# Kernel tuning notes

Measured on AMD Instinct MI355X. Metric: run time of the kernel, lower is better.

The kernel has to match this reference:

```python
import jax, jax.numpy as jnp
import numpy as np

H, D = 4, 32            # heads, per-head dim
HD = H * D              # hidden_dim = output_dim = 128
ND, NG = 10000, 30000   # num disease / gene nodes
E_DG, E_GD, E_GG = 150000, 150000, 300000
L = 2                   # num HGTConv layers


def setup_inputs() -> dict:
    key = jax.random.key(0)
    ks = jax.random.split(key, 16)
    s = 0.05
    return {
        "x_d": jax.random.normal(ks[0], (ND, HD), jnp.float32),
        "x_g": jax.random.normal(ks[1], (NG, HD), jnp.float32),
        "src_dg": jax.random.randint(ks[2], (E_DG,), 0, ND),
        "dst_dg": jax.random.randint(ks[3], (E_DG,), 0, NG),
        "src_gd": jax.random.randint(ks[4], (E_GD,), 0, NG),
        "dst_gd": jax.random.randint(ks[5], (E_GD,), 0, ND),
        "src_gg": jax.random.randint(ks[6], (E_GG,), 0, NG),
        "dst_gg": jax.random.randint(ks[7], (E_GG,), 0, NG),
        # fused K/Q/V projection per node type, stacked over layers
        "Wkqv_d": jax.random.normal(ks[8], (L, HD, 3 * HD), jnp.float32) * s,
        "bkqv_d": jnp.zeros((L, 3 * HD), jnp.float32),
        "Wkqv_g": jax.random.normal(ks[9], (L, HD, 3 * HD), jnp.float32) * s,
        "bkqv_g": jnp.zeros((L, 3 * HD), jnp.float32),
        # output linear per node type
        "Wout_d": jax.random.normal(ks[10], (L, HD, HD), jnp.float32) * s,
        "bout_d": jnp.zeros((L, HD), jnp.float32),
        "Wout_g": jax.random.normal(ks[11], (L, HD, HD), jnp.float32) * s,
        "bout_g": jnp.zeros((L, HD), jnp.float32),
        # learnable skip gates per node type
        "skip_d": jnp.ones((L,), jnp.float32),
        "skip_g": jnp.ones((L,), jnp.float32),
        # per edge-type relation matrices (key, message) and priors, 3 edge types
        "arel": jax.random.normal(ks[12], (L, 3, H, D, D), jnp.float32) * s,
        "mrel": jax.random.normal(ks[13], (L, 3, H, D, D), jnp.float32) * s,
        "prel": jnp.ones((L, 3, H), jnp.float32),
    }


def _hgt_forward(x_d, x_g, src_dg, dst_dg, src_gd, dst_gd, src_gg, dst_gg,
                 Wkqv_d, bkqv_d, Wkqv_g, bkqv_g, Wout_d, bout_d, Wout_g, bout_g,
                 skip_d, skip_g, arel, mrel, prel):
    scale = 1.0 / (D ** 0.5)
    for l in range(L):
        def kqv(x, W, b):
            t = (x @ W + b).reshape(-1, 3, H, D)
            return t[:, 0], t[:, 1], t[:, 2]

        k_d, q_d, v_d = kqv(x_d, Wkqv_d[l], bkqv_d[l])
        k_g, q_g, v_g = kqv(x_g, Wkqv_g[l], bkqv_g[l])

        def edge_msgs(k_src, v_src, q_dst, src, dst, et):
            # gather src K/V, transform by per-edge-type relation matrices
            ke = jnp.einsum('ehd,hdf->ehf', k_src[src], arel[l, et])  # [E,H,D]
            ve = jnp.einsum('ehd,hdf->ehf', v_src[src], mrel[l, et])  # [E,H,D]
            a = jnp.sum(q_dst[dst] * ke, axis=-1) * prel[l, et] * scale  # [E,H]
            return a, ve

        a_dg, v_dg = edge_msgs(k_d, v_d, q_g, src_dg, dst_dg, 0)
        a_gd, v_gd = edge_msgs(k_g, v_g, q_d, src_gd, dst_gd, 1)
        a_gg, v_gg = edge_msgs(k_g, v_g, q_g, src_gg, dst_gg, 2)

        def aggregate(alphas, vals, dsts, n):
            # segment softmax over ALL incoming edges of a dst node (across edge types)
            a = jnp.concatenate(alphas, axis=0)
            v = jnp.concatenate(vals, axis=0)
            d = jnp.concatenate(dsts, axis=0)
            amax = jax.ops.segment_max(a, d, num_segments=n)
            ex = jnp.exp(a - amax[d])
            den = jax.ops.segment_sum(ex, d, num_segments=n)
            w = ex / den[d]
            out = jax.ops.segment_sum(w[:, :, None] * v, d, num_segments=n)
            return out.reshape(n, HD)

        agg_g = aggregate([a_dg, a_gg], [v_dg, v_gg], [dst_dg, dst_gg], NG)
        agg_d = aggregate([a_gd], [v_gd], [dst_gd], ND)

        def update(agg, x, Wout, bout, skip):
            o = jax.nn.gelu(agg) @ Wout + bout
            g = jax.nn.sigmoid(skip)
            return g * o + (1.0 - g) * x

        x_d = update(agg_d, x_d, Wout_d[l], bout_d[l], skip_d[l])
        x_g = update(agg_g, x_g, Wout_g[l], bout_g[l], skip_g[l])
    return x_d, x_g


def reference(x_d, x_g, src_dg, dst_dg, src_gd, dst_gd, src_gg, dst_gg,
              Wkqv_d, bkqv_d, Wkqv_g, bkqv_g, Wout_d, bout_d, Wout_g, bout_g,
              skip_d, skip_g, arel, mrel, prel):
    return _hgt_forward(x_d, x_g, src_dg, dst_dg, src_gd, dst_gd, src_gg, dst_gg,
                        Wkqv_d, bkqv_d, Wkqv_g, bkqv_g, Wout_d, bout_d, Wout_g, bout_g,
                        skip_d, skip_g, arel, mrel, prel)
```

## Files before the change

kernel.cpp:

```cpp
#include <hip/hip_runtime.h>
#include <hip/hip_bf16.h>

#define H 4
#define D 32
#define HD 128
#define ND 10000
#define NG 30000
#define E_DG 150000
#define E_GD 150000
#define E_GG 300000
#define NE (E_DG + E_GD + E_GG)
#define EG (E_DG + E_GG)
#define NLAYER 2
#define NBG 30
#define NBD 10
#define OCG 640
#define OCD 384
#define GOFF ((size_t)ND * OCD)
#define NSCAT 2344
#define NGEMM0 1250
#define XLSTRIDE 136

typedef _Float16 f16;
typedef __attribute__((ext_vector_type(2))) _Float16 f16x2;
typedef __attribute__((ext_vector_type(4))) _Float16 f16x4;
typedef __attribute__((ext_vector_type(8))) _Float16 f16x8;
typedef __attribute__((ext_vector_type(8))) unsigned short u16x8;
typedef __attribute__((ext_vector_type(4))) float f32x4;

__device__ __forceinline__ float bu(unsigned short u) {
    return __uint_as_float(((unsigned)u) << 16);
}
__device__ __forceinline__ float ldraw(const void* p, size_t i, bool isf32) {
    return isf32 ? ((const float*)p)[i] : bu(((const unsigned short*)p)[i]);
}
__device__ __forceinline__ float gelu(float v) {
    const float c = 0.79788456080286536f * (v + 0.044715f * v * v * v);
    return 0.5f * v * (1.0f + tanhf(c));
}

__device__ __forceinline__ void combine_one(
    int idx, int GENE, bool isf32,
    const void* W, const void* bvec,
    const void* arel, const void* mrel, const void* prel,
    f16* __restrict__ Wp, float* __restrict__ bp) {
    const int OC = GENE ? OCG : OCD;
    const int l = idx / (OC * 128);
    const int rem = idx - l * OC * 128;
    const int col = rem >> 7;
    const int d = rem & 127;
    const int g = col >> 7;
    const int jj = col & 127;
    const int h = jj >> 5, f = jj & 31;
    const size_t wbase = (size_t)l * 128 * 384;
    const size_t bbase = (size_t)l * 384;
    float val, bv = 0.f;
    if (g == 0) {
        val = ldraw(W, wbase + d * 384 + 128 + jj, isf32);
        bv = ldraw(bvec, bbase + 128 + jj, isf32);
    } else {
        const int et = GENE ? ((g <= 2) ? 1 : 2) : 0;
        const bool isk = (g & 1);
        const void* mat = isk ? arel : mrel;
        const size_t mbase = (((size_t)(l * 3 + et) * H + h) << 10) + f;
        const int sb = isk ? 0 : 256;
        val = 0.f;
        for (int dd = 0; dd < 32; dd++)
            val += ldraw(W, wbase + d * 384 + sb + h * 32 + dd, isf32) *
                   ldraw(mat, mbase + dd * 32, isf32);
        if (d == 0)
            for (int dd = 0; dd < 32; dd++)
                bv += ldraw(bvec, bbase + sb + h * 32 + dd, isf32) *
                      ldraw(mat, mbase + dd * 32, isf32);
        if (isk) {
            const float sc = ldraw(prel, (size_t)(l * 3 + et) * H + h, isf32) *
                             (0.17677669529663689f * 1.4426950408889634f);
            val *= sc;
            bv *= sc;
        }
    }
    Wp[(size_t)l * 4 * OC * 32 + ((size_t)(d >> 5) * OC + col) * 32 + (d & 31)] = (f16)val;
    if (d == 0) bp[l * OC + col] = bv;
}

__global__ __launch_bounds__(256) void k_prep0(
    const void* x0,
    const void* wkqvd_r, const void* bkqvd_r,
    const void* wkqvg_r, const void* bkqvg_r,
    const void* arel_r, const void* mrel_r, const void* prel_r,
    const void* woutd_r, const void* woutg_r,
    const void* boutd_r, const void* boutg_r,
    const void* skipd_r, const void* skipg_r,
    f16* __restrict__ Wp_d, float* __restrict__ bp_d,
    f16* __restrict__ Wp_g, float* __restrict__ bp_g,
    f16* __restrict__ Wpod, f16* __restrict__ Wpog,
    float* __restrict__ boutc_d, float* __restrict__ boutc_g,
    float* __restrict__ gates, int* __restrict__ flag,
    const int* __restrict__ dst_dg, const int* __restrict__ dst_gg,
    const int* __restrict__ dst_gd,
    int* __restrict__ cnt_g, int* __restrict__ cnt_d,
    int* __restrict__ rank, int* __restrict__ ready) {
    const int tid = threadIdx.x;
    const int b = blockIdx.x;
    if (b >= 1281) {
        const int i = (b - 1281) * 256 + tid;
        if (i < E_DG) rank[i] = atomicAdd(cnt_g + dst_dg[i], 1);
        else if (i < EG) rank[i] = atomicAdd(cnt_g + dst_gg[i - E_DG], 1);
        else if (i < NE) rank[i] = atomicAdd(cnt_d + dst_gd[i - EG], 1);
        return;
    }
    __shared__ int sbad;
    if (tid == 0) sbad = 0;
    __syncthreads();
    {
        const unsigned short* xs = (const unsigned short*)x0;
        int bad = 0;
        for (int i = tid; i < 1024; i += 256)
            if (!(fabsf(bu(xs[i])) < 1e6f)) bad = 1;
        if (bad) sbad = 1;
    }
    __syncthreads();
    const bool isf32 = (sbad != 0);

    if (b < 1280) {
        int idx = b * 256 + tid;
        const int nd = NLAYER * OCD * 128;
        const int ng = NLAYER * OCG * 128;
        const int np = 2 * NLAYER * 128 * 128;
        if (idx < nd) {
            combine_one(idx, 0, isf32, wkqvd_r, bkqvd_r, arel_r, mrel_r, prel_r, Wp_d, bp_d);
        } else if ((idx -= nd) < ng) {
            combine_one(idx, 1, isf32, wkqvg_r, bkqvg_r, arel_r, mrel_r, prel_r, Wp_g, bp_g);
        } else if ((idx -= ng) < np) {
            const int type = idx >= NLAYER * 128 * 128;
            int rem = idx - type * NLAYER * 128 * 128;
            const int l = rem / (128 * 128);
            rem -= l * 128 * 128;
            const int d = rem >> 7, col = rem & 127;
            const float w = ldraw(type ? woutg_r : woutd_r,
                                  (size_t)l * 128 * 128 + d * 128 + col, isf32);
            f16* out = (type ? Wpog : Wpod) +
                ((size_t)l * 4 + (d >> 5)) * 128 * 32 + col * 32 + (d & 31);
            *out = (f16)w;
        }
    } else {
        if (tid < NBG + NBD) ready[tid] = 0;
        if (tid == 0) {
            flag[0] = isf32 ? 1 : 0;
            gates[0] = 1.f / (1.f + expf(-ldraw(skipd_r, 0, isf32)));
            gates[1] = 1.f / (1.f + expf(-ldraw(skipg_r, 0, isf32)));
            gates[2] = 1.f / (1.f + expf(-ldraw(skipd_r, 1, isf32)));
            gates[3] = 1.f / (1.f + expf(-ldraw(skipg_r, 1, isf32)));
        }
        for (int i = tid; i < NLAYER * 128; i += 256) {
            boutc_d[i] = ldraw(boutd_r, i, isf32);
            boutc_g[i] = ldraw(boutg_r, i, isf32);
        }
    }
}

__global__ __launch_bounds__(256) void k_scan(
    const int* __restrict__ cnt_g, const int* __restrict__ cnt_d,
    int* __restrict__ ready,
    int* __restrict__ rp_g, int* __restrict__ rp_d) {
    const int b = blockIdx.x;
    const int tid = threadIdx.x;
    const bool isg = (b < NBG);
    const int* cnt = isg ? cnt_g : cnt_d;
    int* rp = isg ? rp_g : rp_d;
    const int n = isg ? NG : ND;
    const int lb = isg ? b : (b - NBG);
    const int i0 = lb * 1024 + tid * 4;
    int v[4];
    int t = 0;
#pragma unroll
    for (int j = 0; j < 4; j++) {
        v[j] = (i0 + j < n) ? cnt[i0 + j] : 0;
        t += v[j];
    }
    __shared__ int sdata[256];
    __shared__ int red2[256];
    __shared__ int s_off;
    sdata[tid] = t;
    __syncthreads();
    for (int d = 1; d < 256; d <<= 1) {
        const int u = (tid >= d) ? sdata[tid - d] : 0;
        __syncthreads();
        sdata[tid] += u;
        __syncthreads();
    }
    const int total = sdata[255];
    if (tid == 0) atomicExch(&ready[b], total + 1);
    const int p0 = isg ? 0 : NBG;
    const int npred = b - p0;
    int part = 0;
    for (int i = tid; i < npred; i += 256) {
        int vv;
        do { vv = atomicAdd(&ready[p0 + i], 0); } while (vv == 0);
        part += vv - 1;
    }
    red2[tid] = part;
    __syncthreads();
    for (int d = 128; d > 0; d >>= 1) {
        if (tid < d) red2[tid] += red2[tid + d];
        __syncthreads();
    }
    if (tid == 0) s_off = red2[0];
    __syncthreads();
    int run = s_off + sdata[tid] - t;
#pragma unroll
    for (int j = 0; j < 4; j++) {
        if (i0 + j < n) {
            run += v[j];
            rp[i0 + j + 1] = run;
        }
    }
    if (tid == 0 && lb == 0) rp[0] = 0;
}

__global__ __launch_bounds__(256) void k_scatter_gemm0(
    const int* __restrict__ src_dg, const int* __restrict__ dst_dg,
    const int* __restrict__ src_gg, const int* __restrict__ dst_gg,
    const int* __restrict__ src_gd, const int* __restrict__ dst_gd,
    const int* __restrict__ rp_g, const int* __restrict__ rp_d,
    const int* __restrict__ rank,
    int* __restrict__ edges_g, int* __restrict__ edges_d,
    const void* xd_r, const void* xg_r, const int* __restrict__ flag,
    const f16* __restrict__ Wpd, const float* __restrict__ bpd,
    const f16* __restrict__ Wpg, const float* __restrict__ bpg,
    f16* __restrict__ tab) {
    __shared__ f16 xls[32 * XLSTRIDE];
    if (blockIdx.x < NSCAT) {
        const int i = blockIdx.x * 256 + threadIdx.x;
        if (i < E_DG) {
            edges_g[rp_g[dst_dg[i]] + rank[i]] = src_dg[i] * OCD + 128;
        } else if (i < EG) {
            const int j = i - E_DG;
            edges_g[rp_g[dst_gg[j]] + rank[i]] = (int)GOFF + src_gg[j] * OCG + 384;
        } else if (i < NE) {
            const int j = i - EG;
            edges_d[rp_d[dst_gd[j]] + rank[i]] = (int)GOFF + src_gd[j] * OCG + 128;
        }
        return;
    }
    const bool isf32 = (*flag != 0);
    const int tid = threadIdx.x;
    const int mt0 = (blockIdx.x - NSCAT) * 2;
    for (int i = tid; i < 1024; i += 256) {
        const int row = i >> 5;
        const int c4 = (i & 31) * 4;
        const int gnode = mt0 * 16 + row;
        const bool gene = (gnode >= ND);
        const void* xr = gene ? xg_r : xd_r;
        const size_t base = (size_t)(gene ? gnode - ND : gnode) * 128 + c4;
        float4 v;
        if (isf32) {
            v = *(const float4*)((const float*)xr + base);
        } else {
            const ushort4 u = *(const ushort4*)((const unsigned short*)xr + base);
            v = make_float4(bu(u.x), bu(u.y), bu(u.z), bu(u.w));
        }
        f16* dst = xls + row * XLSTRIDE + c4;
        dst[0] = (f16)v.x; dst[1] = (f16)v.y; dst[2] = (f16)v.z; dst[3] = (f16)v.w;
    }
    __syncthreads();

    const int wv = tid >> 6, lane = tid & 63;
    const int r = lane & 15, q4 = lane >> 4;
    const int n0 = (mt0 * 16 >= ND) ? 10 : 6;
    const int n1 = ((mt0 + 1) * 16 >= ND) ? 10 : 6;
    for (int it = wv; it < n0 + n1; it += 4) {
        const int mtl = (it < n0) ? 0 : 1;
        const int ntl = (it < n0) ? it : (it - n0);
        const int node0 = (mt0 + mtl) * 16;
        const bool gene = (node0 >= ND);
        const int OC = gene ? OCG : OCD;
        const f16* Wp = gene ? Wpg : Wpd;
        const float* bias = gene ? bpg : bpd;
        f16* out = gene ? (tab + GOFF) : tab;
        const int trow0 = node0 - (gene ? ND : 0);
        const int col0 = ntl << 6;
        f32x4 acc0 = {0.f, 0.f, 0.f, 0.f};
        f32x4 acc1 = acc0, acc2 = acc0, acc3 = acc0;
#pragma unroll
        for (int kb = 0; kb < 4; kb++) {
            const f16x8 a = *(const f16x8*)(xls + (mtl * 16 + r) * XLSTRIDE + kb * 32 + q4 * 8);
            const f16* wb = Wp + ((size_t)kb * OC + col0 + r) * 32 + q4 * 8;
            const f16x8 b0 = *(const f16x8*)(wb);
            const f16x8 b1 = *(const f16x8*)(wb + 512);
            const f16x8 b2 = *(const f16x8*)(wb + 1024);
            const f16x8 b3 = *(const f16x8*)(wb + 1536);
            acc0 = __builtin_amdgcn_mfma_f32_16x16x32_f16(b0, a, acc0, 0, 0, 0);
            acc1 = __builtin_amdgcn_mfma_f32_16x16x32_f16(b1, a, acc1, 0, 0, 0);
            acc2 = __builtin_amdgcn_mfma_f32_16x16x32_f16(b2, a, acc2, 0, 0, 0);
            acc3 = __builtin_amdgcn_mfma_f32_16x16x32_f16(b3, a, acc3, 0, 0, 0);
        }
        const f32x4 accs[4] = {acc0, acc1, acc2, acc3};
#pragma unroll
        for (int t = 0; t < 4; t++) {
            const int col = col0 + t * 16 + q4 * 4;
            const f32x4 bb = *(const f32x4*)(bias + col);
            f16x4 o;
#pragma unroll
            for (int reg = 0; reg < 4; reg++)
                o[reg] = (f16)(accs[t][reg] + bb[reg]);
            *(f16x4*)(out + (size_t)(trow0 + r) * OC + col) = o;
        }
    }
}

__global__ __launch_bounds__(256) void k_agg(
    const int* __restrict__ rp_g, const int* __restrict__ edges_g,
    const int* __restrict__ rp_d, const int* __restrict__ edges_d,
    const f16* __restrict__ tab, f16* __restrict__ gagg) {
    const int wid = blockIdx.x * 4 + (threadIdx.x >> 6);
    const int lane = threadIdx.x & 63;
    const int slot = lane >> 4, sub = lane & 15;

    int node, row;
    const int *rp, *edges;
    size_t qoff;
    if (wid < NG) {
        node = wid; rp = rp_g; edges = edges_g;
        qoff = GOFF + (size_t)node * OCG;
        row = ND + node;
    } else {
        node = wid - NG; rp = rp_d; edges = edges_d;
        qoff = (size_t)node * OCD;
        row = node;
    }

    union U { f16x8 v; f16x2 p[4]; };
    U q;
    q.v = *(const f16x8*)(tab + qoff + sub * 8);

    float s = 0.f;
    float acc[8];
#pragma unroll
    for (int i = 0; i < 8; i++) acc[i] = 0.f;

    const int r0 = rp[node], r1 = rp[node + 1];
    int e = r0 + slot;

    auto kvload = [&](int rec, U& k, U& v) {
        const f16* p = tab + (size_t)rec + sub * 8;
        k.v = *(const f16x8*)p;
        v.v = *(const f16x8*)(p + 128);
    };

    int recA0 = (e < r1) ? edges[e] : 0;
    int recB0 = (e + 4 < r1) ? edges[e + 4] : 0;
    U kA0, vA0, kB0, vB0;
    kvload(recA0, kA0, vA0);
    kvload(recB0, kB0, vB0);
    int recA1 = (e + 8 < r1) ? edges[e + 8] : 0;
    int recB1 = (e + 12 < r1) ? edges[e + 12] : 0;

    while (e < r1) {
        const int recA2 = (e + 16 < r1) ? edges[e + 16] : 0;
        const int recB2 = (e + 20 < r1) ? edges[e + 20] : 0;
        U kA1, vA1, kB1, vB1;
        kvload(recA1, kA1, vA1);
        kvload(recB1, kB1, vB1);

        float pA = __builtin_amdgcn_fdot2(q.p[0], kA0.p[0], 0.f, false);
        float pB = __builtin_amdgcn_fdot2(q.p[0], kB0.p[0], 0.f, false);
        pA = __builtin_amdgcn_fdot2(q.p[1], kA0.p[1], pA, false);
        pB = __builtin_amdgcn_fdot2(q.p[1], kB0.p[1], pB, false);
        pA = __builtin_amdgcn_fdot2(q.p[2], kA0.p[2], pA, false);
        pB = __builtin_amdgcn_fdot2(q.p[2], kB0.p[2], pB, false);
        pA = __builtin_amdgcn_fdot2(q.p[3], kA0.p[3], pA, false);
        pB = __builtin_amdgcn_fdot2(q.p[3], kB0.p[3], pB, false);
        pA += __shfl_xor(pA, 1);
        pB += __shfl_xor(pB, 1);
        pA += __shfl_xor(pA, 2);
        pB += __shfl_xor(pB, 2);
        const float eaA = exp2f(pA);
        const float eaB = (e + 4 < r1) ? exp2f(pB) : 0.f;
        s += eaA + eaB;
#pragma unroll
        for (int i = 0; i < 8; i++)
            acc[i] = fmaf(eaB, (float)vB0.v[i], fmaf(eaA, (float)vA0.v[i], acc[i]));
        recA0 = recA1; recB0 = recB1; recA1 = recA2; recB1 = recB2;
        kA0 = kA1; vA0 = vA1; kB0 = kB1; vB0 = vB1;
        e += 8;
    }

#pragma unroll
    for (int mask = 16; mask <= 32; mask <<= 1) {
        s += __shfl_xor(s, mask);
#pragma unroll
        for (int i = 0; i < 8; i++) acc[i] += __shfl_xor(acc[i], mask);
    }

    const float inv = (s > 0.f) ? (1.f / s) : 0.f;
    if (slot == 0) {
        f16x8 o;
#pragma unroll
        for (int i = 0; i < 8; i++) o[i] = (f16)gelu(acc[i] * inv);
        *(f16x8*)(gagg + (size_t)row * HD + sub * 8) = o;
    }
}

__global__ __launch_bounds__(256) void k_updgemm(
    const f16* __restrict__ gagg,
    const f16* __restrict__ Wpod0, const f16* __restrict__ Wpog0,
    const float* __restrict__ boutc_d0, const float* __restrict__ boutc_g0,
    const float* __restrict__ gates,
    const void* xd_r, const void* xg_r, const int* __restrict__ flag,
    f16* __restrict__ xball,
    const f16* __restrict__ Wpd1, const float* __restrict__ bpd1,
    const f16* __restrict__ Wpg1, const float* __restrict__ bpg1,
    f16* __restrict__ tab) {
    __shared__ f16 xls[32 * XLSTRIDE];
    const bool isf32 = (*flag != 0);
    const int tid = threadIdx.x;
    const int wv = tid >> 6, lane = tid & 63;
    const int r = lane & 15, q4 = lane >> 4;

    {
        const int mtl = wv >> 1, nt = wv & 1;
        const int mtile = blockIdx.x * 2 + mtl;
        const int node0 = mtile * 16;
        const bool gene = (node0 >= ND);
        const f16* Wp = gene ? Wpog0 : Wpod0;
        const float* bias = gene ? boutc_g0 : boutc_d0;
        const float g = gates[gene ? 1 : 0];
        const int col0 = nt << 6;
        f32x4 acc0 = {0.f, 0.f, 0.f, 0.f};
        f32x4 acc1 = acc0, acc2 = acc0, acc3 = acc0;
#pragma unroll
        for (int kb = 0; kb < 4; kb++) {
            const f16x8 a = *(const f16x8*)(gagg + (size_t)(node0 + r) * 128 + kb * 32 + q4 * 8);
            const f16* wb = Wp + ((size_t)kb * 128 + col0 + r) * 32 + q4 * 8;
            const f16x8 b0 = *(const f16x8*)(wb);
            const f16x8 b1 = *(const f16x8*)(wb + 512);
            const f16x8 b2 = *(const f16x8*)(wb + 1024);
            const f16x8 b3 = *(const f16x8*)(wb + 1536);
            acc0 = __builtin_amdgcn_mfma_f32_16x16x32_f16(b0, a, acc0, 0, 0, 0);
            acc1 = __builtin_amdgcn_mfma_f32_16x16x32_f16(b1, a, acc1, 0, 0, 0);
            acc2 = __builtin_amdgcn_mfma_f32_16x16x32_f16(b2, a, acc2, 0, 0, 0);
            acc3 = __builtin_amdgcn_mfma_f32_16x16x32_f16(b3, a, acc3, 0, 0, 0);
        }
        const f32x4 accs[4] = {acc0, acc1, acc2, acc3};
        const void* xr = gene ? xg_r : xd_r;
        const int lrow0 = node0 - (gene ? ND : 0);
#pragma unroll
        for (int t = 0; t < 4; t++) {
            const int col = col0 + t * 16 + q4 * 4;
            const f32x4 bb = *(const f32x4*)(bias + col);
            const size_t xbase = (size_t)(lrow0 + r) * 128 + col;
            float xo[4];
            if (isf32) {
                const f32x4 u = *(const f32x4*)((const float*)xr + xbase);
#pragma unroll
                for (int reg = 0; reg < 4; reg++) xo[reg] = u[reg];
            } else {
                const ushort4 u = *(const ushort4*)((const unsigned short*)xr + xbase);
                xo[0] = bu(u.x); xo[1] = bu(u.y); xo[2] = bu(u.z); xo[3] = bu(u.w);
            }
            f16x4 xv;
#pragma unroll
            for (int reg = 0; reg < 4; reg++) {
                const float xn = g * (accs[t][reg] + bb[reg]) + (1.f - g) * xo[reg];
                xv[reg] = (f16)xn;
            }
            *(f16x4*)(xls + (mtl * 16 + r) * XLSTRIDE + col) = xv;
            *(f16x4*)(xball + (size_t)(node0 + r) * 128 + col) = xv;
        }
    }
    __syncthreads();

    const int mt0 = blockIdx.x * 2;
    const int n0 = ((mt0 * 16) >= ND) ? 10 : 6;
    const int n1 = (((mt0 + 1) * 16) >= ND) ? 10 : 6;
    for (int it = wv; it < n0 + n1; it += 4) {
        const int mtl = (it < n0) ? 0 : 1;
        const int ntl = (it < n0) ? it : (it - n0);
        const int node0 = (mt0 + mtl) * 16;
        const bool gene = (node0 >= ND);
        const int OC = gene ? OCG : OCD;
        const f16* Wp = gene ? Wpg1 : Wpd1;
        const float* bias = gene ? bpg1 : bpd1;
        f16* out = gene ? (tab + GOFF) : tab;
        const int trow0 = node0 - (gene ? ND : 0);
        const int col0 = ntl << 6;
        f32x4 acc0 = {0.f, 0.f, 0.f, 0.f};
        f32x4 acc1 = acc0, acc2 = acc0, acc3 = acc0;
#pragma unroll
        for (int kb = 0; kb < 4; kb++) {
            const f16x8 a = *(const f16x8*)(xls + (mtl * 16 + r) * XLSTRIDE + kb * 32 + q4 * 8);
            const f16* wb = Wp + ((size_t)kb * OC + col0 + r) * 32 + q4 * 8;
            const f16x8 b0 = *(const f16x8*)(wb);
            const f16x8 b1 = *(const f16x8*)(wb + 512);
            const f16x8 b2 = *(const f16x8*)(wb + 1024);
            const f16x8 b3 = *(const f16x8*)(wb + 1536);
            acc0 = __builtin_amdgcn_mfma_f32_16x16x32_f16(b0, a, acc0, 0, 0, 0);
            acc1 = __builtin_amdgcn_mfma_f32_16x16x32_f16(b1, a, acc1, 0, 0, 0);
            acc2 = __builtin_amdgcn_mfma_f32_16x16x32_f16(b2, a, acc2, 0, 0, 0);
            acc3 = __builtin_amdgcn_mfma_f32_16x16x32_f16(b3, a, acc3, 0, 0, 0);
        }
        const f32x4 accs[4] = {acc0, acc1, acc2, acc3};
#pragma unroll
        for (int t = 0; t < 4; t++) {
            const int col = col0 + t * 16 + q4 * 4;
            const f32x4 bb = *(const f32x4*)(bias + col);
            f16x4 o;
#pragma unroll
            for (int reg = 0; reg < 4; reg++)
                o[reg] = (f16)(accs[t][reg] + bb[reg]);
            *(f16x4*)(out + (size_t)(trow0 + r) * OC + col) = o;
        }
    }
}

__global__ __launch_bounds__(256) void k_upd1(
    const f16* __restrict__ gagg,
    const f16* __restrict__ Wpod1, const f16* __restrict__ Wpog1,
    const float* __restrict__ boutc_d1, const float* __restrict__ boutc_g1,
    const float* __restrict__ gates,
    const f16* __restrict__ xball, float* __restrict__ dout) {
    const int w = blockIdx.x * 4 + (threadIdx.x >> 6);
    const int nt = w / 2500, mt = w - nt * 2500;
    const int node0 = mt << 4;
    const bool gene = (node0 >= ND);
    const f16* Wp = gene ? Wpog1 : Wpod1;
    const float* bias = gene ? boutc_g1 : boutc_d1;
    const float g = gates[gene ? 1 : 0];
    const int lane = threadIdx.x & 63;
    const int r = lane & 15, q4 = lane >> 4;
    const int col0 = nt << 6;
    f32x4 acc0 = {0.f, 0.f, 0.f, 0.f};
    f32x4 acc1 = acc0, acc2 = acc0, acc3 = acc0;
#pragma unroll
    for (int kb = 0; kb < 4; kb++) {
        const f16x8 a = *(const f16x8*)(gagg + (size_t)(node0 + r) * 128 + kb * 32 + q4 * 8);
        const f16* wb = Wp + ((size_t)kb * 128 + col0 + r) * 32 + q4 * 8;
        const f16x8 b0 = *(const f16x8*)(wb);
        const f16x8 b1 = *(const f16x8*)(wb + 512);
        const f16x8 b2 = *(const f16x8*)(wb + 1024);
        const f16x8 b3 = *(const f16x8*)(wb + 1536);
        acc0 = __builtin_amdgcn_mfma_f32_16x16x32_f16(b0, a, acc0, 0, 0, 0);
        acc1 = __builtin_amdgcn_mfma_f32_16x16x32_f16(b1, a, acc1, 0, 0, 0);
        acc2 = __builtin_amdgcn_mfma_f32_16x16x32_f16(b2, a, acc2, 0, 0, 0);
        acc3 = __builtin_amdgcn_mfma_f32_16x16x32_f16(b3, a, acc3, 0, 0, 0);
    }
    const f32x4 accs[4] = {acc0, acc1, acc2, acc3};
#pragma unroll
    for (int t = 0; t < 4; t++) {
        const int col = col0 + t * 16 + q4 * 4;
        const f32x4 bb = *(const f32x4*)(bias + col);
        const size_t idx = (size_t)(node0 + r) * 128 + col;
        const f16x4 xb = *(const f16x4*)(xball + idx);
        f32x4 o;
#pragma unroll
        for (int reg = 0; reg < 4; reg++)
            o[reg] = g * (accs[t][reg] + bb[reg]) + (1.f - g) * (float)xb[reg];
        *(f32x4*)(dout + idx) = o;
    }
}

static inline size_t alignup(size_t v) { return (v + 15) & ~(size_t)15; }

extern "C" void kernel_launch(void* const* d_in, const int* in_sizes, int n_in,
                              void* d_out, int out_size, void* d_ws, size_t ws_size,
                              hipStream_t stream) {
    (void)in_sizes; (void)n_in; (void)out_size; (void)ws_size;
    const int* src_dg = (const int*)d_in[2];
    const int* dst_dg = (const int*)d_in[3];
    const int* src_gd = (const int*)d_in[4];
    const int* dst_gd = (const int*)d_in[5];
    const int* src_gg = (const int*)d_in[6];
    const int* dst_gg = (const int*)d_in[7];

    float* ws = (float*)d_ws;
    int* flag = (int*)ws; ws += 16;
    int* cnt_g  = (int*)ws; ws += alignup(NG);
    int* cnt_d  = (int*)ws; ws += alignup(ND);
    int* rp_g   = (int*)ws; ws += alignup(NG + 1);
    int* rp_d   = (int*)ws; ws += alignup(ND + 1);
    int* rank   = (int*)ws; ws += alignup(NE);
    int* ready  = (int*)ws; ws += 64;
    int* edges_g = (int*)ws; ws += alignup(EG);
    int* edges_d = (int*)ws; ws += alignup(E_GD);
    float* bp_d = ws; ws += alignup((size_t)NLAYER * OCD);
    float* bp_g = ws; ws += alignup((size_t)NLAYER * OCG);
    float* boutc_d = ws; ws += alignup((size_t)NLAYER * 128);
    float* boutc_g = ws; ws += alignup((size_t)NLAYER * 128);
    float* gates = ws; ws += 16;
    f16* Wp_d = (f16*)ws; ws += alignup((size_t)NLAYER * 4 * OCD * 32 / 2);
    f16* Wp_g = (f16*)ws; ws += alignup((size_t)NLAYER * 4 * OCG * 32 / 2);
    f16* Wpod = (f16*)ws; ws += alignup((size_t)NLAYER * 4 * 128 * 32 / 2);
    f16* Wpog = (f16*)ws; ws += alignup((size_t)NLAYER * 4 * 128 * 32 / 2);
    f16* xball = (f16*)ws; ws += alignup((size_t)(ND + NG) * HD / 2);
    f16* gagg  = (f16*)ws; ws += alignup((size_t)(ND + NG) * HD / 2);
    f16* tab   = (f16*)ws; ws += alignup(((size_t)ND * OCD + (size_t)NG * OCG) / 2);

    hipMemsetAsync(cnt_g, 0, (size_t)(NG + ND) * sizeof(int), stream);
    k_prep0<<<1281 + NSCAT, 256, 0, stream>>>(
        d_in[0],
        d_in[8], d_in[9], d_in[10], d_in[11],
        d_in[18], d_in[19], d_in[20],
        d_in[12], d_in[14], d_in[13], d_in[15], d_in[16], d_in[17],
        Wp_d, bp_d, Wp_g, bp_g, Wpod, Wpog, boutc_d, boutc_g,
        gates, flag,
        dst_dg, dst_gg, dst_gd, cnt_g, cnt_d, rank, ready);
    k_scan<<<NBG + NBD, 256, 0, stream>>>(cnt_g, cnt_d, ready, rp_g, rp_d);
    k_scatter_gemm0<<<NSCAT + NGEMM0, 256, 0, stream>>>(
        src_dg, dst_dg, src_gg, dst_gg, src_gd, dst_gd,
        rp_g, rp_d, rank, edges_g, edges_d,
        d_in[0], d_in[1], flag,
        Wp_d, bp_d, Wp_g, bp_g, tab);
    k_agg<<<(NG + ND) / 4, 256, 0, stream>>>(rp_g, edges_g, rp_d, edges_d, tab, gagg);
    k_updgemm<<<(ND + NG) / 32, 256, 0, stream>>>(
        gagg, Wpod, Wpog, boutc_d, boutc_g, gates,
        d_in[0], d_in[1], flag, xball,
        Wp_d + (size_t)4 * OCD * 32, bp_d + OCD,
        Wp_g + (size_t)4 * OCG * 32, bp_g + OCG, tab);
    k_agg<<<(NG + ND) / 4, 256, 0, stream>>>(rp_g, edges_g, rp_d, edges_d, tab, gagg);
    k_upd1<<<(ND + NG) / 32, 256, 0, stream>>>(
        gagg, Wpod + (size_t)4 * 128 * 32, Wpog + (size_t)4 * 128 * 32,
        boutc_d + 128, boutc_g + 128, gates + 2, xball, (float*)d_out);
}
```

Measured before the change: 333.7 us.

## Merge scan with layer-0 KQV GEMM and cache weight fragments across four m-tiles

The prefix scan now runs in the same launch as the layer-0 KQV projection, and the edge scatter becomes its own kernel. The GEMM blocks grow from two to four 16-row m-tiles, so each wave loads its weight fragments into registers once and reuses them across the tiles. The same register-resident weight reuse is applied to the update GEMMs. This should cut redundant global weight loads and one launch boundary, at the cost of higher register pressure, fewer blocks, and scan blocks that spin-wait inside a larger grid.

```diff
diff --git a/kernel.cpp b/kernel.cpp
--- a/kernel.cpp
+++ b/kernel.cpp
@@ -14,18 +14,18 @@
 #define NLAYER 2
 #define NBG 30
 #define NBD 10
+#define NSCAN (NBG + NBD)
 #define OCG 640
 #define OCD 384
 #define GOFF ((size_t)ND * OCD)
 #define NSCAT 2344
-#define NGEMM0 1250
+#define NQUAD 625
 #define XLSTRIDE 136
 
 typedef _Float16 f16;
 typedef __attribute__((ext_vector_type(2))) _Float16 f16x2;
 typedef __attribute__((ext_vector_type(4))) _Float16 f16x4;
 typedef __attribute__((ext_vector_type(8))) _Float16 f16x8;
-typedef __attribute__((ext_vector_type(8))) unsigned short u16x8;
 typedef __attribute__((ext_vector_type(4))) float f32x4;
 
 __device__ __forceinline__ float bu(unsigned short u) {
@@ -144,7 +144,7 @@
             *out = (f16)w;
         }
     } else {
-        if (tid < NBG + NBD) ready[tid] = 0;
+        if (tid < NSCAN) ready[tid] = 0;
         if (tid == 0) {
             flag[0] = isf32 ? 1 : 0;
             gates[0] = 1.f / (1.f + expf(-ldraw(skipd_r, 0, isf32)));
@@ -159,94 +159,162 @@
     }
 }
 
-__global__ __launch_bounds__(256) void k_scan(
+__device__ __forceinline__ void kqv_block_4mt(
+    const f16* xls, int tid, int mt0,
+    const f16* __restrict__ Wpd, const float* __restrict__ bpd,
+    const f16* __restrict__ Wpg, const float* __restrict__ bpg,
+    f16* __restrict__ tab) {
+    const int wv = tid >> 6, lane = tid & 63;
+    const int r = lane & 15, q4 = lane >> 4;
+    const bool g0 = (mt0 * 16 >= ND);
+    const bool g3 = ((mt0 + 3) * 16 >= ND);
+    if (g0 == g3) {
+        const bool gene = g0;
+        const int OC = gene ? OCG : OCD;
+        const f16* Wp = gene ? Wpg : Wpd;
+        const float* bias = gene ? bpg : bpd;
+        f16* out = gene ? (tab + GOFF) : tab;
+        const int trow0 = mt0 * 16 - (gene ? ND : 0);
+        const int nt = gene ? 10 : 6;
+        for (int ntl = wv; ntl < nt; ntl += 4) {
+            const int col0 = ntl << 6;
+            f16x8 B[4][4];
+#pragma unroll
+            for (int kb = 0; kb < 4; kb++) {
+                const f16* wb = Wp + ((size_t)kb * OC + col0 + r) * 32 + q4 * 8;
+#pragma unroll
+                for (int t = 0; t < 4; t++) B[kb][t] = *(const f16x8*)(wb + t * 512);
+            }
+#pragma unroll 1
+            for (int mtl = 0; mtl < 4; mtl++) {
+                f32x4 acc[4];
+                acc[0] = acc[1] = acc[2] = acc[3] = (f32x4){0.f, 0.f, 0.f, 0.f};
+#pragma unroll
+                for (int kb = 0; kb < 4; kb++) {
+                    const f16x8 a = *(const f16x8*)(xls + (mtl * 16 + r) * XLSTRIDE + kb * 32 + q4 * 8);
+#pragma unroll
+                    for (int t = 0; t < 4; t++)
+                        acc[t] = __builtin_amdgcn_mfma_f32_16x16x32_f16(B[kb][t], a, acc[t], 0, 0, 0);
+                }
+#pragma unroll
+                for (int t = 0; t < 4; t++) {
+                    const int col = col0 + t * 16 + q4 * 4;
+                    const f32x4 bb = *(const f32x4*)(bias + col);
+                    f16x4 o;
+#pragma unroll
+                    for (int reg = 0; reg < 4; reg++)
+                        o[reg] = (f16)(acc[t][reg] + bb[reg]);
+                    *(f16x4*)(out + (size_t)(trow0 + mtl * 16 + r) * OC + col) = o;
+                }
+            }
+        }
+    } else {
+        for (int mtl = 0; mtl < 4; mtl++) {
+            const int node0 = (mt0 + mtl) * 16;
+            const bool gene = (node0 >= ND);
+            const int OC = gene ? OCG : OCD;
+            const f16* Wp = gene ? Wpg : Wpd;
+            const float* bias = gene ? bpg : bpd;
+            f16* out = gene ? (tab + GOFF) : tab;
+            const int trow0 = node0 - (gene ? ND : 0);
+            const int nt = gene ? 10 : 6;
+            for (int ntl = wv; ntl < nt; ntl += 4) {
+                const int col0 = ntl << 6;
+                f32x4 acc[4];
+                acc[0] = acc[1] = acc[2] = acc[3] = (f32x4){0.f, 0.f, 0.f, 0.f};
+#pragma unroll
+                for (int kb = 0; kb < 4; kb++) {
+                    const f16x8 a = *(const f16x8*)(xls + (mtl * 16 + r) * XLSTRIDE + kb * 32 + q4 * 8);
+                    const f16* wb = Wp + ((size_t)kb * OC + col0 + r) * 32 + q4 * 8;
+#pragma unroll
+                    for (int t = 0; t < 4; t++) {
+                        const f16x8 bt = *(const f16x8*)(wb + t * 512);
+                        acc[t] = __builtin_amdgcn_mfma_f32_16x16x32_f16(bt, a, acc[t], 0, 0, 0);
+                    }
+                }
+#pragma unroll
+                for (int t = 0; t < 4; t++) {
+                    const int col = col0 + t * 16 + q4 * 4;
+                    const f32x4 bb = *(const f32x4*)(bias + col);
+                    f16x4 o;
+#pragma unroll
+                    for (int reg = 0; reg < 4; reg++)
+                        o[reg] = (f16)(acc[t][reg] + bb[reg]);
+                    *(f16x4*)(out + (size_t)(trow0 + r) * OC + col) = o;
+                }
+            }
+        }
+    }
+}
+
+__global__ __launch_bounds__(256) void k_scangemm0(
     const int* __restrict__ cnt_g, const int* __restrict__ cnt_d,
     int* __restrict__ ready,
-    int* __restrict__ rp_g, int* __restrict__ rp_d) {
-    const int b = blockIdx.x;
-    const int tid = threadIdx.x;
-    const bool isg = (b < NBG);
-    const int* cnt = isg ? cnt_g : cnt_d;
-    int* rp = isg ? rp_g : rp_d;
-    const int n = isg ? NG : ND;
-    const int lb = isg ? b : (b - NBG);
-    const int i0 = lb * 1024 + tid * 4;
-    int v[4];
-    int t = 0;
-#pragma unroll
-    for (int j = 0; j < 4; j++) {
-        v[j] = (i0 + j < n) ? cnt[i0 + j] : 0;
-        t += v[j];
-    }
-    __shared__ int sdata[256];
-    __shared__ int red2[256];
-    __shared__ int s_off;
-    sdata[tid] = t;
-    __syncthreads();
-    for (int d = 1; d < 256; d <<= 1) {
-        const int u = (tid >= d) ? sdata[tid - d] : 0;
-        __syncthreads();
-        sdata[tid] += u;
-        __syncthreads();
-    }
-    const int total = sdata[255];
-    if (tid == 0) atomicExch(&ready[b], total + 1);
-    const int p0 = isg ? 0 : NBG;
-    const int npred = b - p0;
-    int part = 0;
-    for (int i = tid; i < npred; i += 256) {
-        int vv;
-        do { vv = atomicAdd(&ready[p0 + i], 0); } while (vv == 0);
-        part += vv - 1;
-    }
-    red2[tid] = part;
-    __syncthreads();
-    for (int d = 128; d > 0; d >>= 1) {
-        if (tid < d) red2[tid] += red2[tid + d];
-        __syncthreads();
-    }
-    if (tid == 0) s_off = red2[0];
-    __syncthreads();
-    int run = s_off + sdata[tid] - t;
-#pragma unroll
-    for (int j = 0; j < 4; j++) {
-        if (i0 + j < n) {
-            run += v[j];
-            rp[i0 + j + 1] = run;
-        }
-    }
-    if (tid == 0 && lb == 0) rp[0] = 0;
-}
-
-__global__ __launch_bounds__(256) void k_scatter_gemm0(
-    const int* __restrict__ src_dg, const int* __restrict__ dst_dg,
-    const int* __restrict__ src_gg, const int* __restrict__ dst_gg,
-    const int* __restrict__ src_gd, const int* __restrict__ dst_gd,
-    const int* __restrict__ rp_g, const int* __restrict__ rp_d,
-    const int* __restrict__ rank,
-    int* __restrict__ edges_g, int* __restrict__ edges_d,
+    int* __restrict__ rp_g, int* __restrict__ rp_d,
     const void* xd_r, const void* xg_r, const int* __restrict__ flag,
     const f16* __restrict__ Wpd, const float* __restrict__ bpd,
     const f16* __restrict__ Wpg, const float* __restrict__ bpg,
     f16* __restrict__ tab) {
-    __shared__ f16 xls[32 * XLSTRIDE];
-    if (blockIdx.x < NSCAT) {
-        const int i = blockIdx.x * 256 + threadIdx.x;
-        if (i < E_DG) {
-            edges_g[rp_g[dst_dg[i]] + rank[i]] = src_dg[i] * OCD + 128;
-        } else if (i < EG) {
-            const int j = i - E_DG;
-            edges_g[rp_g[dst_gg[j]] + rank[i]] = (int)GOFF + src_gg[j] * OCG + 384;
-        } else if (i < NE) {
-            const int j = i - EG;
-            edges_d[rp_d[dst_gd[j]] + rank[i]] = (int)GOFF + src_gd[j] * OCG + 128;
-        }
+    __shared__ int sdata[256];
+    __shared__ int red2[256];
+    __shared__ int s_off;
+    __shared__ f16 xls[64 * XLSTRIDE];
+    const int tid = threadIdx.x;
+    if (blockIdx.x < NSCAN) {
+        const int b = blockIdx.x;
+        const bool isg = (b < NBG);
+        const int* cnt = isg ? cnt_g : cnt_d;
+        int* rp = isg ? rp_g : rp_d;
+        const int n = isg ? NG : ND;
+        const int lb = isg ? b : (b - NBG);
+        const int i0 = lb * 1024 + tid * 4;
+        int v[4];
+        int t = 0;
+#pragma unroll
+        for (int j = 0; j < 4; j++) {
+            v[j] = (i0 + j < n) ? cnt[i0 + j] : 0;
+            t += v[j];
+        }
+        sdata[tid] = t;
+        __syncthreads();
+        for (int d = 1; d < 256; d <<= 1) {
+            const int u = (tid >= d) ? sdata[tid - d] : 0;
+            __syncthreads();
+            sdata[tid] += u;
+            __syncthreads();
+        }
+        const int total = sdata[255];
+        if (tid == 0) atomicExch(&ready[b], total + 1);
+        const int p0 = isg ? 0 : NBG;
+        const int npred = b - p0;
+        int part = 0;
+        for (int i = tid; i < npred; i += 256) {
+            int vv;
+            do { vv = atomicAdd(&ready[p0 + i], 0); } while (vv == 0);
+            part += vv - 1;
+        }
+        red2[tid] = part;
+        __syncthreads();
+        for (int d = 128; d > 0; d >>= 1) {
+            if (tid < d) red2[tid] += red2[tid + d];
+            __syncthreads();
+        }
+        if (tid == 0) s_off = red2[0];
+        __syncthreads();
+        int run = s_off + sdata[tid] - t;
+#pragma unroll
+        for (int j = 0; j < 4; j++) {
+            if (i0 + j < n) {
+                run += v[j];
+                rp[i0 + j + 1] = run;
+            }
+        }
+        if (tid == 0 && lb == 0) rp[0] = 0;
         return;
     }
     const bool isf32 = (*flag != 0);
-    const int tid = threadIdx.x;
-    const int mt0 = (blockIdx.x - NSCAT) * 2;
-    for (int i = tid; i < 1024; i += 256) {
+    const int mt0 = (blockIdx.x - NSCAN) * 4;
+    for (int i = tid; i < 2048; i += 256) {
         const int row = i >> 5;
         const int c4 = (i & 31) * 4;
         const int gnode = mt0 * 16 + row;
@@ -264,48 +332,25 @@
         dst[0] = (f16)v.x; dst[1] = (f16)v.y; dst[2] = (f16)v.z; dst[3] = (f16)v.w;
     }
     __syncthreads();
-
-    const int wv = tid >> 6, lane = tid & 63;
-    const int r = lane & 15, q4 = lane >> 4;
-    const int n0 = (mt0 * 16 >= ND) ? 10 : 6;
-    const int n1 = ((mt0 + 1) * 16 >= ND) ? 10 : 6;
-    for (int it = wv; it < n0 + n1; it += 4) {
-        const int mtl = (it < n0) ? 0 : 1;
-        const int ntl = (it < n0) ? it : (it - n0);
-        const int node0 = (mt0 + mtl) * 16;
-        const bool gene = (node0 >= ND);
-        const int OC = gene ? OCG : OCD;
-        const f16* Wp = gene ? Wpg : Wpd;
-        const float* bias = gene ? bpg : bpd;
-        f16* out = gene ? (tab + GOFF) : tab;
-        const int trow0 = node0 - (gene ? ND : 0);
-        const int col0 = ntl << 6;
-        f32x4 acc0 = {0.f, 0.f, 0.f, 0.f};
-        f32x4 acc1 = acc0, acc2 = acc0, acc3 = acc0;
-#pragma unroll
-        for (int kb = 0; kb < 4; kb++) {
-            const f16x8 a = *(const f16x8*)(xls + (mtl * 16 + r) * XLSTRIDE + kb * 32 + q4 * 8);
-            const f16* wb = Wp + ((size_t)kb * OC + col0 + r) * 32 + q4 * 8;
-            const f16x8 b0 = *(const f16x8*)(wb);
-            const f16x8 b1 = *(const f16x8*)(wb + 512);
-            const f16x8 b2 = *(const f16x8*)(wb + 1024);
-            const f16x8 b3 = *(const f16x8*)(wb + 1536);
-            acc0 = __builtin_amdgcn_mfma_f32_16x16x32_f16(b0, a, acc0, 0, 0, 0);
-            acc1 = __builtin_amdgcn_mfma_f32_16x16x32_f16(b1, a, acc1, 0, 0, 0);
-            acc2 = __builtin_amdgcn_mfma_f32_16x16x32_f16(b2, a, acc2, 0, 0, 0);
-            acc3 = __builtin_amdgcn_mfma_f32_16x16x32_f16(b3, a, acc3, 0, 0, 0);
-        }
-        const f32x4 accs[4] = {acc0, acc1, acc2, acc3};
-#pragma unroll
-        for (int t = 0; t < 4; t++) {
-            const int col = col0 + t * 16 + q4 * 4;
-            const f32x4 bb = *(const f32x4*)(bias + col);
-            f16x4 o;
-#pragma unroll
-            for (int reg = 0; reg < 4; reg++)
-                o[reg] = (f16)(accs[t][reg] + bb[reg]);
-            *(f16x4*)(out + (size_t)(trow0 + r) * OC + col) = o;
-        }
+    kqv_block_4mt(xls, tid, mt0, Wpd, bpd, Wpg, bpg, tab);
+}
+
+__global__ __launch_bounds__(256) void k_scatter(
+    const int* __restrict__ src_dg, const int* __restrict__ dst_dg,
+    const int* __restrict__ src_gg, const int* __restrict__ dst_gg,
+    const int* __restrict__ src_gd, const int* __restrict__ dst_gd,
+    const int* __restrict__ rp_g, const int* __restrict__ rp_d,
+    const int* __restrict__ rank,
+    int* __restrict__ edges_g, int* __restrict__ edges_d) {
+    const int i = blockIdx.x * 256 + threadIdx.x;
+    if (i < E_DG) {
+        edges_g[rp_g[dst_dg[i]] + rank[i]] = src_dg[i] * OCD + 128;
+    } else if (i < EG) {
+        const int j = i - E_DG;
+        edges_g[rp_g[dst_gg[j]] + rank[i]] = (int)GOFF + src_gg[j] * OCG + 384;
+    } else if (i < NE) {
+        const int j = i - EG;
+        edges_d[rp_d[dst_gd[j]] + rank[i]] = (int)GOFF + src_gd[j] * OCG + 128;
     }
 }
 
@@ -412,106 +457,72 @@
     const f16* __restrict__ Wpd1, const float* __restrict__ bpd1,
     const f16* __restrict__ Wpg1, const float* __restrict__ bpg1,
     f16* __restrict__ tab) {
-    __shared__ f16 xls[32 * XLSTRIDE];
+    __shared__ f16 xls[64 * XLSTRIDE];
     const bool isf32 = (*flag != 0);
     const int tid = threadIdx.x;
     const int wv = tid >> 6, lane = tid & 63;
     const int r = lane & 15, q4 = lane >> 4;
 
     {
-        const int mtl = wv >> 1, nt = wv & 1;
-        const int mtile = blockIdx.x * 2 + mtl;
-        const int node0 = mtile * 16;
-        const bool gene = (node0 >= ND);
-        const f16* Wp = gene ? Wpog0 : Wpod0;
-        const float* bias = gene ? boutc_g0 : boutc_d0;
-        const float g = gates[gene ? 1 : 0];
-        const int col0 = nt << 6;
-        f32x4 acc0 = {0.f, 0.f, 0.f, 0.f};
-        f32x4 acc1 = acc0, acc2 = acc0, acc3 = acc0;
-#pragma unroll
-        for (int kb = 0; kb < 4; kb++) {
-            const f16x8 a = *(const f16x8*)(gagg + (size_t)(node0 + r) * 128 + kb * 32 + q4 * 8);
-            const f16* wb = Wp + ((size_t)kb * 128 + col0 + r) * 32 + q4 * 8;
-            const f16x8 b0 = *(const f16x8*)(wb);
-            const f16x8 b1 = *(const f16x8*)(wb + 512);
-            const f16x8 b2 = *(const f16x8*)(wb + 1024);
-            const f16x8 b3 = *(const f16x8*)(wb + 1536);
-            acc0 = __builtin_amdgcn_mfma_f32_16x16x32_f16(b0, a, acc0, 0, 0, 0);
-            acc1 = __builtin_amdgcn_mfma_f32_16x16x32_f16(b1, a, acc1, 0, 0, 0);
-            acc2 = __builtin_amdgcn_mfma_f32_16x16x32_f16(b2, a, acc2, 0, 0, 0);
-            acc3 = __builtin_amdgcn_mfma_f32_16x16x32_f16(b3, a, acc3, 0, 0, 0);
-        }
-        const f32x4 accs[4] = {acc0, acc1, acc2, acc3};
-        const void* xr = gene ? xg_r : xd_r;
-        const int lrow0 = node0 - (gene ? ND : 0);
-#pragma unroll
-        for (int t = 0; t < 4; t++) {
-            const int col = col0 + t * 16 + q4 * 4;
-            const f32x4 bb = *(const f32x4*)(bias + col);
-            const size_t xbase = (size_t)(lrow0 + r) * 128 + col;
-            float xo[4];
-            if (isf32) {
-                const f32x4 u = *(const f32x4*)((const float*)xr + xbase);
-#pragma unroll
-                for (int reg = 0; reg < 4; reg++) xo[reg] = u[reg];
-            } else {
-                const ushort4 u = *(const ushort4*)((const unsigned short*)xr + xbase);
-                xo[0] = bu(u.x); xo[1] = bu(u.y); xo[2] = bu(u.z); xo[3] = bu(u.w);
-            }
-            f16x4 xv;
-#pragma unroll
-            for (int reg = 0; reg < 4; reg++) {
-                const float xn = g * (accs[t][reg] + bb[reg]) + (1.f - g) * xo[reg];
-                xv[reg] = (f16)xn;
-            }
-            *(f16x4*)(xls + (mtl * 16 + r) * XLSTRIDE + col) = xv;
-            *(f16x4*)(xball + (size_t)(node0 + r) * 128 + col) = xv;
+        const int nt = wv & 1, col0 = nt << 6;
+        f16x8 B[4][4];
+        int prevg = -1;
+#pragma unroll 1
+        for (int p = 0; p < 2; p++) {
+            const int mtl = (wv >> 1) + p * 2;
+            const int node0 = (blockIdx.x * 4 + mtl) * 16;
+            const bool gene = (node0 >= ND);
+            const f16* Wp = gene ? Wpog0 : Wpod0;
+            const float* bias = gene ? boutc_g0 : boutc_d0;
+            const float g = gates[gene ? 1 : 0];
+            if ((int)gene != prevg) {
+                prevg = (int)gene;
+#pragma unroll
+                for (int kb = 0; kb < 4; kb++) {
+                    const f16* wb = Wp + ((size_t)kb * 128 + col0 + r) * 32 + q4 * 8;
+#pragma unroll
+                    for (int t = 0; t < 4; t++) B[kb][t] = *(const f16x8*)(wb + t * 512);
+                }
+            }
+            f32x4 acc[4];
+            acc[0] = acc[1] = acc[2] = acc[3] = (f32x4){0.f, 0.f, 0.f, 0.f};
+#pragma unroll
+            for (int kb = 0; kb < 4; kb++) {
+                const f16x8 a = *(const f16x8*)(gagg + (size_t)(node0 + r) * 128 + kb * 32 + q4 * 8);
+#pragma unroll
+                for (int t = 0; t < 4; t++)
+                    acc[t] = __builtin_amdgcn_mfma_f32_16x16x32_f16(B[kb][t], a, acc[t], 0, 0, 0);
+            }
+            const void* xr = gene ? xg_r : xd_r;
+            const int lrow0 = node0 - (gene ? ND : 0);
+#pragma unroll
+            for (int t = 0; t < 4; t++) {
+                const int col = col0 + t * 16 + q4 * 4;
+                const f32x4 bb = *(const f32x4*)(bias + col);
+                const size_t xbase = (size_t)(lrow0 + r) * 128 + col;
+                float xo[4];
+                if (isf32) {
+                    const f32x4 u = *(const f32x4*)((const float*)xr + xbase);
+#pragma unroll
+                    for (int reg = 0; reg < 4; reg++) xo[reg] = u[reg];
+                } else {
+                    const ushort4 u = *(const ushort4*)((const unsigned short*)xr + xbase);
+                    xo[0] = bu(u.x); xo[1] = bu(u.y); xo[2] = bu(u.z); xo[3] = bu(u.w);
+                }
+                f16x4 xv;
+#pragma unroll
+                for (int reg = 0; reg < 4; reg++) {
+                    const float xn = g * (acc[t][reg] + bb[reg]) + (1.f - g) * xo[reg];
+                    xv[reg] = (f16)xn;
+                }
+                *(f16x4*)(xls + (mtl * 16 + r) * XLSTRIDE + col) = xv;
+                *(f16x4*)(xball + (size_t)(node0 + r) * 128 + col) = xv;
+            }
         }
     }
     __syncthreads();
 
-    const int mt0 = blockIdx.x * 2;
-    const int n0 = ((mt0 * 16) >= ND) ? 10 : 6;
-    const int n1 = (((mt0 + 1) * 16) >= ND) ? 10 : 6;
-    for (int it = wv; it < n0 + n1; it += 4) {
-        const int mtl = (it < n0) ? 0 : 1;
-        const int ntl = (it < n0) ? it : (it - n0);
-        const int node0 = (mt0 + mtl) * 16;
-        const bool gene = (node0 >= ND);
-        const int OC = gene ? OCG : OCD;
-        const f16* Wp = gene ? Wpg1 : Wpd1;
-        const float* bias = gene ? bpg1 : bpd1;
-        f16* out = gene ? (tab + GOFF) : tab;
-        const int trow0 = node0 - (gene ? ND : 0);
-        const int col0 = ntl << 6;
-        f32x4 acc0 = {0.f, 0.f, 0.f, 0.f};
-        f32x4 acc1 = acc0, acc2 = acc0, acc3 = acc0;
-#pragma unroll
-        for (int kb = 0; kb < 4; kb++) {
-            const f16x8 a = *(const f16x8*)(xls + (mtl * 16 + r) * XLSTRIDE + kb * 32 + q4 * 8);
-            const f16* wb = Wp + ((size_t)kb * OC + col0 + r) * 32 + q4 * 8;
-            const f16x8 b0 = *(const f16x8*)(wb);
-            const f16x8 b1 = *(const f16x8*)(wb + 512);
-            const f16x8 b2 = *(const f16x8*)(wb + 1024);
-            const f16x8 b3 = *(const f16x8*)(wb + 1536);
-            acc0 = __builtin_amdgcn_mfma_f32_16x16x32_f16(b0, a, acc0, 0, 0, 0);
-            acc1 = __builtin_amdgcn_mfma_f32_16x16x32_f16(b1, a, acc1, 0, 0, 0);
-            acc2 = __builtin_amdgcn_mfma_f32_16x16x32_f16(b2, a, acc2, 0, 0, 0);
-            acc3 = __builtin_amdgcn_mfma_f32_16x16x32_f16(b3, a, acc3, 0, 0, 0);
-        }
-        const f32x4 accs[4] = {acc0, acc1, acc2, acc3};
-#pragma unroll
-        for (int t = 0; t < 4; t++) {
-            const int col = col0 + t * 16 + q4 * 4;
-            const f32x4 bb = *(const f32x4*)(bias + col);
-            f16x4 o;
-#pragma unroll
-            for (int reg = 0; reg < 4; reg++)
-                o[reg] = (f16)(accs[t][reg] + bb[reg]);
-            *(f16x4*)(out + (size_t)(trow0 + r) * OC + col) = o;
-        }
-    }
+    kqv_block_4mt(xls, tid, blockIdx.x * 4, Wpd1, bpd1, Wpg1, bpg1, tab);
 }
 
 __global__ __launch_bounds__(256) void k_upd1(
@@ -520,43 +531,50 @@
     const float* __restrict__ boutc_d1, const float* __restrict__ boutc_g1,
     const float* __restrict__ gates,
     const f16* __restrict__ xball, float* __restrict__ dout) {
-    const int w = blockIdx.x * 4 + (threadIdx.x >> 6);
-    const int nt = w / 2500, mt = w - nt * 2500;
-    const int node0 = mt << 4;
-    const bool gene = (node0 >= ND);
-    const f16* Wp = gene ? Wpog1 : Wpod1;
-    const float* bias = gene ? boutc_g1 : boutc_d1;
-    const float g = gates[gene ? 1 : 0];
-    const int lane = threadIdx.x & 63;
+    const int tid = threadIdx.x;
+    const int wv = tid >> 6, lane = tid & 63;
     const int r = lane & 15, q4 = lane >> 4;
-    const int col0 = nt << 6;
-    f32x4 acc0 = {0.f, 0.f, 0.f, 0.f};
-    f32x4 acc1 = acc0, acc2 = acc0, acc3 = acc0;
-#pragma unroll
-    for (int kb = 0; kb < 4; kb++) {
-        const f16x8 a = *(const f16x8*)(gagg + (size_t)(node0 + r) * 128 + kb * 32 + q4 * 8);
-        const f16* wb = Wp + ((size_t)kb * 128 + col0 + r) * 32 + q4 * 8;
-        const f16x8 b0 = *(const f16x8*)(wb);
-        const f16x8 b1 = *(const f16x8*)(wb + 512);
-        const f16x8 b2 = *(const f16x8*)(wb + 1024);
-        const f16x8 b3 = *(const f16x8*)(wb + 1536);
-        acc0 = __builtin_amdgcn_mfma_f32_16x16x32_f16(b0, a, acc0, 0, 0, 0);
-        acc1 = __builtin_amdgcn_mfma_f32_16x16x32_f16(b1, a, acc1, 0, 0, 0);
-        acc2 = __builtin_amdgcn_mfma_f32_16x16x32_f16(b2, a, acc2, 0, 0, 0);
-        acc3 = __builtin_amdgcn_mfma_f32_16x16x32_f16(b3, a, acc3, 0, 0, 0);
-    }
-    const f32x4 accs[4] = {acc0, acc1, acc2, acc3};
-#pragma unroll
-    for (int t = 0; t < 4; t++) {
-        const int col = col0 + t * 16 + q4 * 4;
-        const f32x4 bb = *(const f32x4*)(bias + col);
-        const size_t idx = (size_t)(node0 + r) * 128 + col;
-        const f16x4 xb = *(const f16x4*)(xball + idx);
-        f32x4 o;
-#pragma unroll
-        for (int reg = 0; reg < 4; reg++)
-            o[reg] = g * (accs[t][reg] + bb[reg]) + (1.f - g) * (float)xb[reg];
-        *(f32x4*)(dout + idx) = o;
+    const int nt = wv & 1, col0 = nt << 6;
+    f16x8 B[4][4];
+    int prevg = -1;
+#pragma unroll 1
+    for (int p = 0; p < 2; p++) {
+        const int mtile = blockIdx.x * 4 + (wv >> 1) * 2 + p;
+        const int node0 = mtile * 16;
+        const bool gene = (node0 >= ND);
+        const f16* Wp = gene ? Wpog1 : Wpod1;
+        const float* bias = gene ? boutc_g1 : boutc_d1;
+        const float g = gates[gene ? 1 : 0];
+        if ((int)gene != prevg) {
+            prevg = (int)gene;
+#pragma unroll
+            for (int kb = 0; kb < 4; kb++) {
+                const f16* wb = Wp + ((size_t)kb * 128 + col0 + r) * 32 + q4 * 8;
+#pragma unroll
+                for (int t = 0; t < 4; t++) B[kb][t] = *(const f16x8*)(wb + t * 512);
+            }
+        }
+        f32x4 acc[4];
+        acc[0] = acc[1] = acc[2] = acc[3] = (f32x4){0.f, 0.f, 0.f, 0.f};
+#pragma unroll
+        for (int kb = 0; kb < 4; kb++) {
+            const f16x8 a = *(const f16x8*)(gagg + (size_t)(node0 + r) * 128 + kb * 32 + q4 * 8);
+#pragma unroll
+            for (int t = 0; t < 4; t++)
+                acc[t] = __builtin_amdgcn_mfma_f32_16x16x32_f16(B[kb][t], a, acc[t], 0, 0, 0);
+        }
+#pragma unroll
+        for (int t = 0; t < 4; t++) {
+            const int col = col0 + t * 16 + q4 * 4;
+            const f32x4 bb = *(const f32x4*)(bias + col);
+            const size_t idx = (size_t)(node0 + r) * 128 + col;
+            const f16x4 xb = *(const f16x4*)(xball + idx);
+            f32x4 o;
+#pragma unroll
+            for (int reg = 0; reg < 4; reg++)
+                o[reg] = g * (acc[t][reg] + bb[reg]) + (1.f - g) * (float)xb[reg];
+            *(f32x4*)(dout + idx) = o;
+        }
     }
 }
 
@@ -605,20 +623,21 @@
         Wp_d, bp_d, Wp_g, bp_g, Wpod, Wpog, boutc_d, boutc_g,
         gates, flag,
         dst_dg, dst_gg, dst_gd, cnt_g, cnt_d, rank, ready);
-    k_scan<<<NBG + NBD, 256, 0, stream>>>(cnt_g, cnt_d, ready, rp_g, rp_d);
-    k_scatter_gemm0<<<NSCAT + NGEMM0, 256, 0, stream>>>(
-        src_dg, dst_dg, src_gg, dst_gg, src_gd, dst_gd,
-        rp_g, rp_d, rank, edges_g, edges_d,
+    k_scangemm0<<<NSCAN + NQUAD, 256, 0, stream>>>(
+        cnt_g, cnt_d, ready, rp_g, rp_d,
         d_in[0], d_in[1], flag,
         Wp_d, bp_d, Wp_g, bp_g, tab);
+    k_scatter<<<NSCAT, 256, 0, stream>>>(
+        src_dg, dst_dg, src_gg, dst_gg, src_gd, dst_gd,
+        rp_g, rp_d, rank, edges_g, edges_d);
     k_agg<<<(NG + ND) / 4, 256, 0, stream>>>(rp_g, edges_g, rp_d, edges_d, tab, gagg);
-    k_updgemm<<<(ND + NG) / 32, 256, 0, stream>>>(
+    k_updgemm<<<NQUAD, 256, 0, stream>>>(
         gagg, Wpod, Wpog, boutc_d, boutc_g, gates,
         d_in[0], d_in[1], flag, xball,
         Wp_d + (size_t)4 * OCD * 32, bp_d + OCD,
         Wp_g + (size_t)4 * OCG * 32, bp_g + OCG, tab);
     k_agg<<<(NG + ND) / 4, 256, 0, stream>>>(rp_g, edges_g, rp_d, edges_d, tab, gagg);
-    k_upd1<<<(ND + NG) / 32, 256, 0, stream>>>(
+    k_upd1<<<NQUAD, 256, 0, stream>>>(
         gagg, Wpod + (size_t)4 * 128 * 32, Wpog + (size_t)4 * 128 * 32,
         boutc_d + 128, boutc_g + 128, gates + 2, xball, (float*)d_out);
 }
```

Measured after the change: 305.5 us. 1.09x faster.
